# Kernel tuning notes

Measured on AMD Instinct MI355X. Metric: run time of the kernel, lower is better.

## Reference

```python
import jax, jax.numpy as jnp
import numpy as np

B = 8192
D_IN = 1024
H = 1024
N_LAYERS = 10  # 1 input layer + 9 hidden layers, then output layer H->1


def setup_inputs() -> dict:
    key = jax.random.key(0)
    ks = jax.random.split(key, 7)
    s_in = 1.0 / np.sqrt(D_IN)
    s_h = 1.0 / np.sqrt(H)
    return {
        "x": jax.random.normal(ks[0], (B, D_IN), dtype=jnp.float32),
        "W0": jax.random.normal(ks[1], (H, D_IN), dtype=jnp.float32) * s_in,
        "b0": jax.random.normal(ks[2], (H,), dtype=jnp.float32) * s_in,
        "Wh": jax.random.normal(ks[3], (N_LAYERS - 1, H, H), dtype=jnp.float32) * s_h,
        "bh": jax.random.normal(ks[4], (N_LAYERS - 1, H), dtype=jnp.float32) * s_h,
        "Wout": jax.random.normal(ks[5], (1, H), dtype=jnp.float32) * s_h,
        "bout": jax.random.normal(ks[6], (1,), dtype=jnp.float32) * s_h,
    }


def reference(x, W0, b0, Wh, bh, Wout, bout):
    # First layer: Linear(D_IN -> H) + sigmoid. torch Linear is x @ W.T + b.
    h = jax.nn.sigmoid(x @ W0.T + b0)  # [B, H]

    # Remaining num_layers-1 hidden layers, identical shape -> lax.scan over stacked weights.
    def step(h, wb):
        W, b = wb
        return jax.nn.sigmoid(h @ W.T + b), None

    h, _ = jax.lax.scan(step, h, (Wh, bh))

    # Output layer: Linear(H -> 1), no activation.
    return h @ Wout.T + bout  # [B, 1]
```

## Files before the change

### kernel.cpp

```cpp
#include <hip/hip_runtime.h>
#include <stdint.h>

typedef unsigned short u16;
typedef unsigned int   u32;
typedef _Float16 f16;
typedef __attribute__((ext_vector_type(4))) float    f32x4;
typedef __attribute__((ext_vector_type(8))) _Float16 f16x8;
typedef __attribute__((ext_vector_type(4))) _Float16 f16x4;

#define DIM    1024
#define NROWS  8192
#define NLAYER 10

__device__ __forceinline__ void gl_lds16(const void* g, void* l) {
    __builtin_amdgcn_global_load_lds((const __attribute__((address_space(1))) u32*)g,
                                     (__attribute__((address_space(3))) u32*)l, 16, 0, 0);
}

__global__ __launch_bounds__(256) void conv_weights(const float* __restrict__ W0,
                                                    const float* __restrict__ Wh,
                                                    f16* __restrict__ Wf) {
    int i = (blockIdx.x * 256 + threadIdx.x) * 4;
    const float* src = (i < 1048576) ? (W0 + i) : (Wh + (i - 1048576));
    float4 w = *(const float4*)src;
    f16x4 o;
    o.x = (f16)w.x; o.y = (f16)w.y; o.z = (f16)w.z; o.w = (f16)w.w;
    *(f16x4*)(Wf + i) = o;
}

__global__ __launch_bounds__(256) void conv_x(const float* __restrict__ x,
                                              f16* __restrict__ Af) {
    int i = (blockIdx.x * 256 + threadIdx.x) * 4;
    float4 w = *(const float4*)(x + i);
    f16x4 o;
    o.x = (f16)w.x; o.y = (f16)w.y; o.z = (f16)w.z; o.w = (f16)w.w;
    *(f16x4*)(Af + i) = o;
}

#define ABUF_B 0
#define BBUF_B 32768
#define BUFSZ  49152
#define NKT    16

__global__ __launch_bounds__(512, 2) void layer_gemm(
        const f16* __restrict__ A,
        const f16* __restrict__ Bg,
        const float* __restrict__ bias,
        f16* __restrict__ O) {
    __shared__ char lds[3 * BUFSZ];

    int bid = blockIdx.x;
    int swz = (bid & 7) * 32 + (bid >> 3);
    int bn = swz & 7;
    int bm = swz >> 3;

    const int tid  = threadIdx.x;
    const int lane = tid & 63;
    const int wid  = tid >> 6;
    const int wr   = wid >> 1;
    const int wc   = wid & 1;

    const int swcol = (((lane & 7) ^ ((lane >> 3) & 7)) << 4);
    const char* gsrc[6];
    u32 ldst[6];
    #pragma unroll
    for (int j = 0; j < 6; ++j) {
        int c = wid * 6 + j;
        if (c < 32) {
            int grow = bm * 256 + c * 8 + (lane >> 3);
            gsrc[j] = (const char*)A + (size_t)grow * 2048 + swcol;
            ldst[j] = ABUF_B + c * 1024;
        } else {
            int c2 = c - 32;
            int grow = bn * 128 + c2 * 8 + (lane >> 3);
            gsrc[j] = (const char*)Bg + (size_t)grow * 2048 + swcol;
            ldst[j] = BBUF_B + c2 * 1024;
        }
    }

    f32x4 acc[4][4];
    #pragma unroll
    for (int mf = 0; mf < 4; ++mf)
        #pragma unroll
        for (int nf = 0; nf < 4; ++nf)
            acc[mf][nf] = (f32x4){0.f, 0.f, 0.f, 0.f};

    #pragma unroll
    for (int j = 0; j < 6; ++j)
        gl_lds16(gsrc[j], lds + ldst[j]);
    #pragma unroll
    for (int j = 0; j < 6; ++j)
        gl_lds16(gsrc[j] + 128, lds + BUFSZ + ldst[j]);

    int cur = 0, nx2 = 2;
    for (int kt = 0; kt < NKT; ++kt) {
        if (kt < NKT - 1) asm volatile("s_waitcnt vmcnt(6)" ::: "memory");
        else              asm volatile("s_waitcnt vmcnt(0)" ::: "memory");
        __builtin_amdgcn_s_barrier();
        __builtin_amdgcn_sched_barrier(0);

        if (kt < NKT - 2) {
            #pragma unroll
            for (int j = 0; j < 6; ++j)
                gl_lds16(gsrc[j] + (size_t)(kt + 2) * 128, lds + nx2 * BUFSZ + ldst[j]);
        }

        const char* base = lds + cur * BUFSZ;
        #pragma unroll
        for (int ks = 0; ks < 2; ++ks) {
            f16x8 a[4], b[4];
            const int cb = ks * 64 + ((lane >> 4) << 4);
            #pragma unroll
            for (int mf = 0; mf < 4; ++mf) {
                int r = wr * 64 + mf * 16 + (lane & 15);
                int byt = r * 128 + (cb ^ ((r & 7) << 4));
                a[mf] = *(const f16x8*)(base + ABUF_B + byt);
            }
            #pragma unroll
            for (int nf = 0; nf < 4; ++nf) {
                int r = wc * 64 + nf * 16 + (lane & 15);
                int byt = r * 128 + (cb ^ ((r & 7) << 4));
                b[nf] = *(const f16x8*)(base + BBUF_B + byt);
            }
            __builtin_amdgcn_s_setprio(1);
            #pragma unroll
            for (int mf = 0; mf < 4; ++mf)
                #pragma unroll
                for (int nf = 0; nf < 4; ++nf)
                    acc[mf][nf] = __builtin_amdgcn_mfma_f32_16x16x32_f16(b[nf], a[mf], acc[mf][nf], 0, 0, 0);
            __builtin_amdgcn_s_setprio(0);
        }
        cur = (cur == 2) ? 0 : cur + 1;
        nx2 = (nx2 == 2) ? 0 : nx2 + 1;
    }

    #pragma unroll
    for (int nf = 0; nf < 4; ++nf) {
        int gn0 = bn * 128 + wc * 64 + nf * 16 + ((lane >> 4) << 2);
        f32x4 b4 = *(const f32x4*)(bias + gn0);
        #pragma unroll
        for (int mf = 0; mf < 4; ++mf) {
            int gm = bm * 256 + wr * 64 + mf * 16 + (lane & 15);
            f16x4 o;
            #pragma unroll
            for (int j = 0; j < 4; ++j) {
                float z = acc[mf][nf][j] + b4[j];
                o[j] = (f16)(1.0f / (1.0f + __expf(-z)));
            }
            *(f16x4*)(O + (size_t)gm * DIM + gn0) = o;
        }
    }
}

__global__ __launch_bounds__(256) void out_gemv(const f16* __restrict__ A,
                                                const float* __restrict__ Wout,
                                                const float* __restrict__ bout,
                                                float* __restrict__ out) {
    int wid  = threadIdx.x >> 6;
    int lane = threadIdx.x & 63;
    int row  = blockIdx.x * 4 + wid;
    const f16* p = A + (size_t)row * DIM + lane * 16;
    const float* pw = Wout + lane * 16;
    float s = 0.f;
    #pragma unroll
    for (int i = 0; i < 4; ++i) {
        f16x4 h4 = *(const f16x4*)(p + i * 4);
        float4 w4 = *(const float4*)(pw + i * 4);
        s += (float)h4.x * w4.x + (float)h4.y * w4.y + (float)h4.z * w4.z + (float)h4.w * w4.w;
    }
    #pragma unroll
    for (int off = 32; off > 0; off >>= 1)
        s += __shfl_down(s, off);
    if (lane == 0) out[row] = s + bout[0];
}

extern "C" void kernel_launch(void* const* d_in, const int* in_sizes, int n_in,
                              void* d_out, int out_size, void* d_ws, size_t ws_size,
                              hipStream_t stream) {
    const float* x    = (const float*)d_in[0];
    const float* W0   = (const float*)d_in[1];
    const float* b0   = (const float*)d_in[2];
    const float* Wh   = (const float*)d_in[3];
    const float* bh   = (const float*)d_in[4];
    const float* Wout = (const float*)d_in[5];
    const float* bout = (const float*)d_in[6];
    float* out = (float*)d_out;

    f16* ws = (f16*)d_ws;
    f16* Wf = ws;
    f16* A0 = Wf + (size_t)NLAYER * DIM * DIM;
    f16* A1 = A0 + (size_t)NROWS * DIM;

    conv_weights<<<NLAYER * DIM * DIM / 1024, 256, 0, stream>>>(W0, Wh, Wf);
    conv_x<<<NROWS * DIM / 1024, 256, 0, stream>>>(x, A0);

    const f16* in = A0;
    f16* o = A1;
    for (int l = 0; l < NLAYER; ++l) {
        const float* bias = (l == 0) ? b0 : (bh + (size_t)(l - 1) * DIM);
        layer_gemm<<<256, 512, 0, stream>>>(in, Wf + (size_t)l * DIM * DIM, bias, o);
        f16* t = (f16*)in; in = o; o = t;
    }

    out_gemv<<<NROWS / 4, 256, 0, stream>>>(in, Wout, bout, out);
}
```

Baseline: 266.4 us.

## Split GEMM k-tile into two phases interleaving LDS reads, prefetch and MFMA

```diff
diff --git a/kernel.cpp b/kernel.cpp
--- a/kernel.cpp
+++ b/kernel.cpp
@@ -78,6 +78,22 @@
         }
     }
 
+    u32 aoff[2][4], boff[2][4];
+    #pragma unroll
+    for (int ks = 0; ks < 2; ++ks) {
+        const int cb = ks * 64 + ((lane >> 4) << 4);
+        #pragma unroll
+        for (int mf = 0; mf < 4; ++mf) {
+            int r = wr * 64 + mf * 16 + (lane & 15);
+            aoff[ks][mf] = ABUF_B + r * 128 + (cb ^ ((r & 7) << 4));
+        }
+        #pragma unroll
+        for (int nf = 0; nf < 4; ++nf) {
+            int r = wc * 64 + nf * 16 + (lane & 15);
+            boff[ks][nf] = BBUF_B + r * 128 + (cb ^ ((r & 7) << 4));
+        }
+    }
+
     f32x4 acc[4][4];
     #pragma unroll
     for (int mf = 0; mf < 4; ++mf)
@@ -92,43 +108,69 @@
     for (int j = 0; j < 6; ++j)
         gl_lds16(gsrc[j] + 128, lds + BUFSZ + ldst[j]);
 
+    asm volatile("s_waitcnt vmcnt(6)" ::: "memory");
+    __builtin_amdgcn_s_barrier();
+    __builtin_amdgcn_sched_barrier(0);
+
     int cur = 0, nx2 = 2;
     for (int kt = 0; kt < NKT; ++kt) {
-        if (kt < NKT - 1) asm volatile("s_waitcnt vmcnt(6)" ::: "memory");
-        else              asm volatile("s_waitcnt vmcnt(0)" ::: "memory");
+        const char* base = lds + cur * BUFSZ;
+        char* sdst = lds + nx2 * BUFSZ;
+
+        f16x8 a0[4], b0[4];
+        #pragma unroll
+        for (int mf = 0; mf < 4; ++mf) a0[mf] = *(const f16x8*)(base + aoff[0][mf]);
+        #pragma unroll
+        for (int nf = 0; nf < 4; ++nf) b0[nf] = *(const f16x8*)(base + boff[0][nf]);
+        __builtin_amdgcn_sched_barrier(0);
+        if (kt < NKT - 2) {
+            #pragma unroll
+            for (int j = 0; j < 3; ++j)
+                gl_lds16(gsrc[j] + (size_t)(kt + 2) * 128, sdst + ldst[j]);
+        }
+        __builtin_amdgcn_sched_barrier(0);
         __builtin_amdgcn_s_barrier();
-        __builtin_amdgcn_sched_barrier(0);
-
+        asm volatile("s_waitcnt lgkmcnt(0)" ::: "memory");
+        __builtin_amdgcn_sched_barrier(0);
+        __builtin_amdgcn_s_setprio(1);
+        #pragma unroll
+        for (int mf = 0; mf < 4; ++mf)
+            #pragma unroll
+            for (int nf = 0; nf < 4; ++nf)
+                acc[mf][nf] = __builtin_amdgcn_mfma_f32_16x16x32_f16(b0[nf], a0[mf], acc[mf][nf], 0, 0, 0);
+        __builtin_amdgcn_s_setprio(0);
+        __builtin_amdgcn_sched_barrier(0);
+        __builtin_amdgcn_s_barrier();
+
+        f16x8 a1[4], b1[4];
+        #pragma unroll
+        for (int mf = 0; mf < 4; ++mf) a1[mf] = *(const f16x8*)(base + aoff[1][mf]);
+        #pragma unroll
+        for (int nf = 0; nf < 4; ++nf) b1[nf] = *(const f16x8*)(base + boff[1][nf]);
+        __builtin_amdgcn_sched_barrier(0);
         if (kt < NKT - 2) {
             #pragma unroll
-            for (int j = 0; j < 6; ++j)
-                gl_lds16(gsrc[j] + (size_t)(kt + 2) * 128, lds + nx2 * BUFSZ + ldst[j]);
-        }
-
-        const char* base = lds + cur * BUFSZ;
-        #pragma unroll
-        for (int ks = 0; ks < 2; ++ks) {
-            f16x8 a[4], b[4];
-            const int cb = ks * 64 + ((lane >> 4) << 4);
-            #pragma unroll
-            for (int mf = 0; mf < 4; ++mf) {
-                int r = wr * 64 + mf * 16 + (lane & 15);
-                int byt = r * 128 + (cb ^ ((r & 7) << 4));
-                a[mf] = *(const f16x8*)(base + ABUF_B + byt);
-            }
-            #pragma unroll
-            for (int nf = 0; nf < 4; ++nf) {
-                int r = wc * 64 + nf * 16 + (lane & 15);
-                int byt = r * 128 + (cb ^ ((r & 7) << 4));
-                b[nf] = *(const f16x8*)(base + BBUF_B + byt);
-            }
-            __builtin_amdgcn_s_setprio(1);
-            #pragma unroll
-            for (int mf = 0; mf < 4; ++mf)
-                #pragma unroll
-                for (int nf = 0; nf < 4; ++nf)
-                    acc[mf][nf] = __builtin_amdgcn_mfma_f32_16x16x32_f16(b[nf], a[mf], acc[mf][nf], 0, 0, 0);
-            __builtin_amdgcn_s_setprio(0);
+            for (int j = 3; j < 6; ++j)
+                gl_lds16(gsrc[j] + (size_t)(kt + 2) * 128, sdst + ldst[j]);
+        }
+        __builtin_amdgcn_sched_barrier(0);
+        __builtin_amdgcn_s_barrier();
+        asm volatile("s_waitcnt lgkmcnt(0)" ::: "memory");
+        __builtin_amdgcn_sched_barrier(0);
+        __builtin_amdgcn_s_setprio(1);
+        #pragma unroll
+        for (int mf = 0; mf < 4; ++mf)
+            #pragma unroll
+            for (int nf = 0; nf < 4; ++nf)
+                acc[mf][nf] = __builtin_amdgcn_mfma_f32_16x16x32_f16(b1[nf], a1[mf], acc[mf][nf], 0, 0, 0);
+        __builtin_amdgcn_s_setprio(0);
+        __builtin_amdgcn_sched_barrier(0);
+
+        if (kt < NKT - 1) {
+            if (kt < NKT - 2) asm volatile("s_waitcnt vmcnt(6)" ::: "memory");
+            else              asm volatile("s_waitcnt vmcnt(0)" ::: "memory");
+            __builtin_amdgcn_s_barrier();
+            __builtin_amdgcn_sched_barrier(0);
         }
         cur = (cur == 2) ? 0 : cur + 1;
         nx2 = (nx2 == 2) ? 0 : nx2 + 1;
```

Measured after the change: 260.1 us. 2.3% less time.

## Fuse all layers and output GEMV into one persistent kernel with grid barriers

Applied to the files above, without the earlier changes.

```diff
diff --git a/kernel.cpp b/kernel.cpp
--- a/kernel.cpp
+++ b/kernel.cpp
@@ -11,6 +11,7 @@
 #define DIM    1024
 #define NROWS  8192
 #define NLAYER 10
+#define NBLK   256
 
 __device__ __forceinline__ void gl_lds16(const void* g, void* l) {
     __builtin_amdgcn_global_load_lds((const __attribute__((address_space(1))) u32*)g,
@@ -42,12 +43,17 @@
 #define BUFSZ  49152
 #define NKT    16
 
-__global__ __launch_bounds__(512, 2) void layer_gemm(
-        const f16* __restrict__ A,
-        const f16* __restrict__ Bg,
-        const float* __restrict__ bias,
-        f16* __restrict__ O) {
-    __shared__ char lds[3 * BUFSZ];
+__global__ __launch_bounds__(512, 2) void mono_net(
+        const f16* __restrict__ Wf,
+        const float* __restrict__ b0,
+        const float* __restrict__ bh,
+        const float* __restrict__ Wout,
+        const float* __restrict__ bout,
+        f16* __restrict__ bufA,
+        f16* __restrict__ bufB,
+        u32* __restrict__ ctr,
+        float* __restrict__ out) {
+    __shared__ char lds[2 * BUFSZ];
 
     int bid = blockIdx.x;
     int swz = (bid & 7) * 32 + (bid >> 3);
@@ -61,117 +67,124 @@
     const int wc   = wid & 1;
 
     const int swcol = (((lane & 7) ^ ((lane >> 3) & 7)) << 4);
-    const char* gsrc[6];
-    u32 ldst[6];
-    #pragma unroll
-    for (int j = 0; j < 6; ++j) {
-        int c = wid * 6 + j;
-        if (c < 32) {
-            int grow = bm * 256 + c * 8 + (lane >> 3);
-            gsrc[j] = (const char*)A + (size_t)grow * 2048 + swcol;
-            ldst[j] = ABUF_B + c * 1024;
-        } else {
-            int c2 = c - 32;
-            int grow = bn * 128 + c2 * 8 + (lane >> 3);
-            gsrc[j] = (const char*)Bg + (size_t)grow * 2048 + swcol;
-            ldst[j] = BBUF_B + c2 * 1024;
-        }
-    }
-
-    f32x4 acc[4][4];
-    #pragma unroll
-    for (int mf = 0; mf < 4; ++mf)
-        #pragma unroll
-        for (int nf = 0; nf < 4; ++nf)
-            acc[mf][nf] = (f32x4){0.f, 0.f, 0.f, 0.f};
-
-    #pragma unroll
-    for (int j = 0; j < 6; ++j)
-        gl_lds16(gsrc[j], lds + ldst[j]);
-    #pragma unroll
-    for (int j = 0; j < 6; ++j)
-        gl_lds16(gsrc[j] + 128, lds + BUFSZ + ldst[j]);
-
-    int cur = 0, nx2 = 2;
-    for (int kt = 0; kt < NKT; ++kt) {
-        if (kt < NKT - 1) asm volatile("s_waitcnt vmcnt(6)" ::: "memory");
-        else              asm volatile("s_waitcnt vmcnt(0)" ::: "memory");
-        __builtin_amdgcn_s_barrier();
-        __builtin_amdgcn_sched_barrier(0);
-
-        if (kt < NKT - 2) {
+
+    for (int l = 0; l < NLAYER; ++l) {
+        const f16* Ab = (l & 1) ? bufB : bufA;
+        f16*       Ob = (l & 1) ? bufA : bufB;
+        const f16* Wb = Wf + (size_t)l * DIM * DIM;
+        const float* bias = l ? (bh + (size_t)(l - 1) * DIM) : b0;
+
+        const char* gsrc[6];
+        u32 ldst[6];
+        #pragma unroll
+        for (int j = 0; j < 6; ++j) {
+            int c = wid * 6 + j;
+            if (c < 32) {
+                int grow = bm * 256 + c * 8 + (lane >> 3);
+                gsrc[j] = (const char*)Ab + (size_t)grow * 2048 + swcol;
+                ldst[j] = ABUF_B + c * 1024;
+            } else {
+                int c2 = c - 32;
+                int grow = bn * 128 + c2 * 8 + (lane >> 3);
+                gsrc[j] = (const char*)Wb + (size_t)grow * 2048 + swcol;
+                ldst[j] = BBUF_B + c2 * 1024;
+            }
+        }
+
+        f32x4 acc[4][4];
+        #pragma unroll
+        for (int mf = 0; mf < 4; ++mf)
             #pragma unroll
-            for (int j = 0; j < 6; ++j)
-                gl_lds16(gsrc[j] + (size_t)(kt + 2) * 128, lds + nx2 * BUFSZ + ldst[j]);
-        }
-
-        const char* base = lds + cur * BUFSZ;
-        #pragma unroll
-        for (int ks = 0; ks < 2; ++ks) {
-            f16x8 a[4], b[4];
-            const int cb = ks * 64 + ((lane >> 4) << 4);
+            for (int nf = 0; nf < 4; ++nf)
+                acc[mf][nf] = (f32x4){0.f, 0.f, 0.f, 0.f};
+
+        #pragma unroll
+        for (int j = 0; j < 6; ++j)
+            gl_lds16(gsrc[j], lds + ldst[j]);
+        __syncthreads();
+
+        for (int kt = 0; kt < NKT; ++kt) {
+            const char* base = lds + (kt & 1) * BUFSZ;
+            if (kt < NKT - 1) {
+                char* nb = lds + ((kt + 1) & 1) * BUFSZ;
+                #pragma unroll
+                for (int j = 0; j < 6; ++j)
+                    gl_lds16(gsrc[j] + (size_t)(kt + 1) * 128, nb + ldst[j]);
+            }
+
+            #pragma unroll
+            for (int ks = 0; ks < 2; ++ks) {
+                f16x8 a[4], b[4];
+                const int cb = ks * 64 + ((lane >> 4) << 4);
+                #pragma unroll
+                for (int mf = 0; mf < 4; ++mf) {
+                    int r = wr * 64 + mf * 16 + (lane & 15);
+                    int byt = r * 128 + (cb ^ ((r & 7) << 4));
+                    a[mf] = *(const f16x8*)(base + ABUF_B + byt);
+                }
+                #pragma unroll
+                for (int nf = 0; nf < 4; ++nf) {
+                    int r = wc * 64 + nf * 16 + (lane & 15);
+                    int byt = r * 128 + (cb ^ ((r & 7) << 4));
+                    b[nf] = *(const f16x8*)(base + BBUF_B + byt);
+                }
+                __builtin_amdgcn_s_setprio(1);
+                #pragma unroll
+                for (int mf = 0; mf < 4; ++mf)
+                    #pragma unroll
+                    for (int nf = 0; nf < 4; ++nf)
+                        acc[mf][nf] = __builtin_amdgcn_mfma_f32_16x16x32_f16(b[nf], a[mf], acc[mf][nf], 0, 0, 0);
+                __builtin_amdgcn_s_setprio(0);
+            }
+            __syncthreads();
+        }
+
+        #pragma unroll
+        for (int nf = 0; nf < 4; ++nf) {
+            int gn0 = bn * 128 + wc * 64 + nf * 16 + ((lane >> 4) << 2);
+            f32x4 b4 = *(const f32x4*)(bias + gn0);
             #pragma unroll
             for (int mf = 0; mf < 4; ++mf) {
-                int r = wr * 64 + mf * 16 + (lane & 15);
-                int byt = r * 128 + (cb ^ ((r & 7) << 4));
-                a[mf] = *(const f16x8*)(base + ABUF_B + byt);
-            }
-            #pragma unroll
-            for (int nf = 0; nf < 4; ++nf) {
-                int r = wc * 64 + nf * 16 + (lane & 15);
-                int byt = r * 128 + (cb ^ ((r & 7) << 4));
-                b[nf] = *(const f16x8*)(base + BBUF_B + byt);
-            }
-            __builtin_amdgcn_s_setprio(1);
-            #pragma unroll
-            for (int mf = 0; mf < 4; ++mf)
-                #pragma unroll
-                for (int nf = 0; nf < 4; ++nf)
-                    acc[mf][nf] = __builtin_amdgcn_mfma_f32_16x16x32_f16(b[nf], a[mf], acc[mf][nf], 0, 0, 0);
-            __builtin_amdgcn_s_setprio(0);
-        }
-        cur = (cur == 2) ? 0 : cur + 1;
-        nx2 = (nx2 == 2) ? 0 : nx2 + 1;
+                int gm = bm * 256 + wr * 64 + mf * 16 + (lane & 15);
+                f16x4 o;
+                #pragma unroll
+                for (int j = 0; j < 4; ++j) {
+                    float z = acc[mf][nf][j] + b4[j];
+                    o[j] = (f16)(1.0f / (1.0f + __expf(-z)));
+                }
+                *(f16x4*)(Ob + (size_t)gm * DIM + gn0) = o;
+            }
+        }
+
+        __syncthreads();
+        if (tid == 0) {
+            __threadfence();
+            atomicAdd(&ctr[l * 16], 1u);
+            while (__hip_atomic_load(&ctr[l * 16], __ATOMIC_RELAXED,
+                                     __HIP_MEMORY_SCOPE_AGENT) < NBLK)
+                __builtin_amdgcn_s_sleep(2);
+            __threadfence();
+        }
+        __syncthreads();
     }
 
     #pragma unroll
-    for (int nf = 0; nf < 4; ++nf) {
-        int gn0 = bn * 128 + wc * 64 + nf * 16 + ((lane >> 4) << 2);
-        f32x4 b4 = *(const f32x4*)(bias + gn0);
-        #pragma unroll
-        for (int mf = 0; mf < 4; ++mf) {
-            int gm = bm * 256 + wr * 64 + mf * 16 + (lane & 15);
-            f16x4 o;
-            #pragma unroll
-            for (int j = 0; j < 4; ++j) {
-                float z = acc[mf][nf][j] + b4[j];
-                o[j] = (f16)(1.0f / (1.0f + __expf(-z)));
-            }
-            *(f16x4*)(O + (size_t)gm * DIM + gn0) = o;
-        }
+    for (int pass = 0; pass < 4; ++pass) {
+        int row = bid * 32 + pass * 8 + wid;
+        const f16* p = bufA + (size_t)row * DIM + lane * 16;
+        const float* pw = Wout + lane * 16;
+        float s = 0.f;
+        #pragma unroll
+        for (int i = 0; i < 4; ++i) {
+            f16x4 h4 = *(const f16x4*)(p + i * 4);
+            float4 w4 = *(const float4*)(pw + i * 4);
+            s += (float)h4.x * w4.x + (float)h4.y * w4.y + (float)h4.z * w4.z + (float)h4.w * w4.w;
+        }
+        #pragma unroll
+        for (int off = 32; off > 0; off >>= 1)
+            s += __shfl_down(s, off);
+        if (lane == 0) out[row] = s + bout[0];
     }
-}
-
-__global__ __launch_bounds__(256) void out_gemv(const f16* __restrict__ A,
-                                                const float* __restrict__ Wout,
-                                                const float* __restrict__ bout,
-                                                float* __restrict__ out) {
-    int wid  = threadIdx.x >> 6;
-    int lane = threadIdx.x & 63;
-    int row  = blockIdx.x * 4 + wid;
-    const f16* p = A + (size_t)row * DIM + lane * 16;
-    const float* pw = Wout + lane * 16;
-    float s = 0.f;
-    #pragma unroll
-    for (int i = 0; i < 4; ++i) {
-        f16x4 h4 = *(const f16x4*)(p + i * 4);
-        float4 w4 = *(const float4*)(pw + i * 4);
-        s += (float)h4.x * w4.x + (float)h4.y * w4.y + (float)h4.z * w4.z + (float)h4.w * w4.w;
-    }
-    #pragma unroll
-    for (int off = 32; off > 0; off >>= 1)
-        s += __shfl_down(s, off);
-    if (lane == 0) out[row] = s + bout[0];
 }
 
 extern "C" void kernel_launch(void* const* d_in, const int* in_sizes, int n_in,
@@ -190,17 +203,11 @@
     f16* Wf = ws;
     f16* A0 = Wf + (size_t)NLAYER * DIM * DIM;
     f16* A1 = A0 + (size_t)NROWS * DIM;
-
+    u32* ctr = (u32*)(A1 + (size_t)NROWS * DIM);
+
+    hipMemsetAsync(ctr, 0, NLAYER * 16 * sizeof(u32), stream);
     conv_weights<<<NLAYER * DIM * DIM / 1024, 256, 0, stream>>>(W0, Wh, Wf);
     conv_x<<<NROWS * DIM / 1024, 256, 0, stream>>>(x, A0);
 
-    const f16* in = A0;
-    f16* o = A1;
-    for (int l = 0; l < NLAYER; ++l) {
-        const float* bias = (l == 0) ? b0 : (bh + (size_t)(l - 1) * DIM);
-        layer_gemm<<<256, 512, 0, stream>>>(in, Wf + (size_t)l * DIM * DIM, bias, o);
-        f16* t = (f16*)in; in = o; o = t;
-    }
-
-    out_gemv<<<NROWS / 4, 256, 0, stream>>>(in, Wout, bout, out);
-}
+    mono_net<<<NBLK, 512, 0, stream>>>(Wf, b0, bh, Wout, bout, A0, A1, ctr, out);
+}
```

Result: slower. 445.9 us (+67.4%).
